# Kernel tuning notes

Measured on AMD Instinct MI355X. Metric: run time of the kernel, lower is better.

Reference implementation:

```python
import jax, jax.numpy as jnp
import numpy as np

XMIN, XMAX = -16.0, 16.0
ZMIN, ZMAX = -16.0, 16.0
SOFTCLIP_L = 5.0


def ref2mem(traj, Zs, Xs):
    # traj: (B, T, 2) cam (x, z) -> mem pixel coords
    x = (traj[..., 0] - XMIN) / ((XMAX - XMIN) / Xs) - 0.5
    z = (traj[..., 1] - ZMIN) / ((ZMAX - ZMIN) / Zs) - 0.5
    return x, z


def bilinear_sample2d(pm, x, z):
    # pm: (B, C, Z, X); x, z: (B, N) float coords -> (B, C, N)
    B, C, Zs, Xs = pm.shape
    x = jnp.clip(x, 0.0, Xs - 1.0)
    z = jnp.clip(z, 0.0, Zs - 1.0)
    x0 = jnp.floor(x).astype(jnp.int32)
    z0 = jnp.floor(z).astype(jnp.int32)
    x1 = jnp.minimum(x0 + 1, Xs - 1)
    z1 = jnp.minimum(z0 + 1, Zs - 1)
    wx = x - x0.astype(x.dtype)
    wz = z - z0.astype(z.dtype)
    pm_flat = pm.reshape(B, C, Zs * Xs)

    def gather(zi, xi):
        idx = (zi * Xs + xi)[:, None, :]  # (B,1,N)
        return jnp.take_along_axis(pm_flat, jnp.broadcast_to(idx, (B, C, idx.shape[-1])), axis=2)

    v00 = gather(z0, x0); v01 = gather(z0, x1)
    v10 = gather(z1, x0); v11 = gather(z1, x1)
    wx = wx[:, None, :]; wz = wz[:, None, :]
    return (v00 * (1 - wx) * (1 - wz) + v01 * wx * (1 - wz)
            + v10 * (1 - wx) * wz + v11 * wx * wz)


def gru_cell(x, h, W_ih, W_hh, b_ih, b_hh):
    gi = x @ W_ih.T + b_ih
    gh = h @ W_hh.T + b_hh
    i_r, i_z, i_n = jnp.split(gi, 3, axis=1)
    h_r, h_z, h_n = jnp.split(gh, 3, axis=1)
    r = jax.nn.sigmoid(i_r + h_r)
    z = jax.nn.sigmoid(i_z + h_z)
    n = jnp.tanh(i_n + r * h_n)
    return (1.0 - z) * n + z * h


def expm_softclip(sig_raw):
    B = sig_raw.shape[0]
    nrm = jnp.linalg.norm(sig_raw.reshape(B, -1), axis=1)
    denom = jax.nn.logsumexp(jnp.stack([nrm / SOFTCLIP_L, jnp.ones_like(nrm)], axis=-1), axis=-1)
    return sig_raw / denom[:, None, None]


def reference(feat_map, pred_map, noise, traj_past,
              W_ih, W_hh, b_ih, b_hh, past_W, past_b,
              W1, b1, W2, b2, W3, b3):
    B, C, Zf, Xf = feat_map.shape
    Zp, Xp = pred_map.shape[2], pred_map.shape[3]
    T_futu = noise.shape[1]
    H = W_hh.shape[1]
    eye2 = jnp.eye(2, dtype=feat_map.dtype)

    # static feature: max_pool2d k=8 s=8 + past encoding
    pooled = feat_map.reshape(B, C, Zf // 8, 8, Xf // 8, 8).max(axis=(3, 5)).reshape(B, -1)
    past_enc = traj_past.reshape(B, -1) @ past_W.T + past_b
    sta_feat = jnp.concatenate([pooled, past_enc], axis=1)  # (B, 2080)

    def step(carry, noise_t):
        hx, win = carry
        xm, zm = ref2mem(win, Zp, Xp)
        feats = bilinear_sample2d(pred_map, xm, zm).reshape(B, -1)  # (B, 3)
        dyn_feat = jnp.concatenate([feats, win.reshape(B, -1)], axis=1)  # (B, 9)
        hx = gru_cell(dyn_feat, hx, W_ih, W_hh, b_ih, b_hh)
        joint = jnp.concatenate([hx, sta_feat], axis=1)  # (B, 2112)
        h1 = jax.nn.leaky_relu(joint @ W1.T + b1)
        h2 = jax.nn.leaky_relu(h1 @ W2.T + b2)
        pred = h2 @ W3.T + b3  # (B, 6)
        mu = pred[:, :2]
        sig_raw = pred[:, 2:].reshape(B, 2, 2) + 1e-8 * eye2
        sig_raw = expm_softclip(sig_raw)
        sig = jnp.einsum('bij,bkj->bik', sig_raw, sig_raw)
        xdotdot = mu + jnp.sum(sig * noise_t[:, None, :], axis=1)
        x_next = 2.0 * win[:, -1] - win[:, -2] + xdotdot  # verlet, dt=1
        win = jnp.concatenate([win[:, 1:], x_next[:, None]], axis=1)
        return (hx, win), x_next

    hx0 = jnp.zeros((B, H), dtype=feat_map.dtype)
    (_, _), traj_futu = jax.lax.scan(step, (hx0, traj_past), jnp.swapaxes(noise, 0, 1))
    return jnp.swapaxes(traj_futu, 0, 1)  # (B, T_futu, 2)


def setup_inputs():
    key = jax.random.key(0)
    ks = jax.random.split(key, 16)
    B, C, Zf, Xf = 192, 32, 64, 64
    T_futu, T_past, H = 27, 3, 32
    d = {}
    d['feat_map'] = jax.random.normal(ks[0], (B, C, Zf, Xf), jnp.float32)
    d['pred_map'] = jax.random.normal(ks[1], (B, 1, Zf, Xf), jnp.float32)
    d['noise'] = jax.random.normal(ks[2], (B, T_futu, 2), jnp.float32)
    d['traj_past'] = jax.random.normal(ks[3], (B, T_past, 2), jnp.float32) * 4.0
    s = 0.05
    d['W_ih'] = jax.random.normal(ks[4], (3 * H, 9), jnp.float32) * s
    d['W_hh'] = jax.random.normal(ks[5], (3 * H, H), jnp.float32) * s
    d['b_ih'] = jnp.zeros((3 * H,), jnp.float32)
    d['b_hh'] = jnp.zeros((3 * H,), jnp.float32)
    d['past_W'] = jax.random.normal(ks[6], (32, T_past * 2), jnp.float32) * s
    d['past_b'] = jnp.zeros((32,), jnp.float32)
    d['W1'] = jax.random.normal(ks[7], (64, 2112), jnp.float32) * 0.02
    d['b1'] = jnp.zeros((64,), jnp.float32)
    d['W2'] = jax.random.normal(ks[8], (32, 64), jnp.float32) * s
    d['b2'] = jnp.zeros((32,), jnp.float32)
    d['W3'] = jax.random.normal(ks[9], (6, 32), jnp.float32) * s
    d['b3'] = jnp.zeros((6,), jnp.float32)
    return d
```

## Files before the change

kernel.cpp:

```cpp
#include <hip/hip_runtime.h>
#include <hip/hip_bf16.h>
#include <math.h>

typedef unsigned int u32;
typedef __fp16 f16x2 __attribute__((ext_vector_type(2)));
typedef u32 u32x4 __attribute__((ext_vector_type(4)));

#define NB    192
#define NC    32
#define TFUT  27
#define BLOB_F_OFF (NB * 64)

#if __has_builtin(__builtin_amdgcn_rcpf)
#define RCPF(x) __builtin_amdgcn_rcpf(x)
#else
#define RCPF(x) (1.0f / (x))
#endif
#if __has_builtin(__builtin_amdgcn_sqrtf)
#define SQRTF(x) __builtin_amdgcn_sqrtf(x)
#else
#define SQRTF(x) sqrtf(x)
#endif
#if __has_builtin(__builtin_amdgcn_exp2f)
#define EXP2F(x) __builtin_amdgcn_exp2f(x)
#else
#define EXP2F(x) exp2f(x)
#endif
#if __has_builtin(__builtin_amdgcn_logf)
#define LOG2F(x) __builtin_amdgcn_logf(x)
#else
#define LOG2F(x) log2f(x)
#endif

#define LDS_FENCE() asm volatile("" ::: "memory")

__device__ __forceinline__ u32 pk16(float lo, float hi) {
    auto v = __builtin_amdgcn_cvt_pkrtz(lo, hi);
    return __builtin_bit_cast(u32, v);
}
__device__ __forceinline__ float fdot2pk(u32 a, u32 b, float c) {
#if __has_builtin(__builtin_amdgcn_fdot2)
    return __builtin_amdgcn_fdot2(__builtin_bit_cast(f16x2, a),
                                  __builtin_bit_cast(f16x2, b), c, false);
#else
    f16x2 av = __builtin_bit_cast(f16x2, a), bv = __builtin_bit_cast(f16x2, b);
    return c + (float)av[0] * (float)bv[0] + (float)av[1] * (float)bv[1];
#endif
}
__device__ __forceinline__ float rdlf(float v, int lane) {
    return __int_as_float(__builtin_amdgcn_readlane(__float_as_int(v), lane));
}
__device__ __forceinline__ float dpp_xor1(float v) {
    return __int_as_float(__builtin_amdgcn_update_dpp(
        0, __float_as_int(v), 0xB1, 0xF, 0xF, true));
}
__device__ __forceinline__ float perm32hi(float v) {
    int x = __float_as_int(v), y = x;
    asm volatile("v_permlane32_swap_b32 %0, %1" : "+v"(x), "+v"(y));
    return __int_as_float(y);
}
__device__ __forceinline__ float swap32_add(float v) {
    int x = __float_as_int(v), y;
    asm volatile("v_mov_b32 %0, %1" : "=v"(y) : "v"(x));
    asm volatile("v_permlane32_swap_b32 %0, %1" : "+v"(x), "+v"(y));
    return __int_as_float(x) + __int_as_float(y);
}
__device__ __forceinline__ float row32_reduce(float v) {
    v += __int_as_float(__builtin_amdgcn_update_dpp(0, __float_as_int(v), 0x121, 0xF, 0xF, true));
    v += __int_as_float(__builtin_amdgcn_update_dpp(0, __float_as_int(v), 0x122, 0xF, 0xF, true));
    v += __int_as_float(__builtin_amdgcn_update_dpp(0, __float_as_int(v), 0x124, 0xF, 0xF, true));
    v += __int_as_float(__builtin_amdgcn_update_dpp(0, __float_as_int(v), 0x128, 0xF, 0xF, true));
    v += __int_as_float(__builtin_amdgcn_update_dpp(0, __float_as_int(v), 0x142, 0xF, 0xF, false));
    return v;
}
__device__ __forceinline__ float sigmoid_f(float x) {
    return RCPF(1.0f + EXP2F(-1.4426950408889634f * x));
}
__device__ __forceinline__ float tanh_f(float x) {
    return __builtin_fmaf(2.0f, RCPF(1.0f + EXP2F(-2.8853900817779268f * x)), -1.0f);
}

__global__ __launch_bounds__(1024) void k_static(
    const float* __restrict__ feat,
    const float* __restrict__ traj_past,
    const float* __restrict__ past_W,
    const float* __restrict__ past_b,
    const float* __restrict__ W1,
    const float* __restrict__ b1,
    const float* __restrict__ W_ih,
    const float* __restrict__ W_hh,
    const float* __restrict__ b_ih,
    const float* __restrict__ b_hh,
    const float* __restrict__ W2,
    const float* __restrict__ b2,
    const float* __restrict__ W3,
    const float* __restrict__ b3,
    float* __restrict__ ws)
{
    const int b = blockIdx.x;
    const int t = threadIdx.x;

    if (b == NB) {
        if (t >= 64) return;
        const int l = t, m2 = l & 31, h = l >> 5;
        u32* blob = reinterpret_cast<u32*>(ws) + BLOB_F_OFF + (size_t)l * 128;
        #pragma unroll
        for (int k = 0; k < 9; ++k) {
            blob[k]     = __float_as_uint(W_ih[l * 9 + k]);
            blob[9 + k] = __float_as_uint(W_ih[(64 + m2) * 9 + k]);
        }
        #pragma unroll
        for (int j = 0; j < 16; ++j) {
            blob[18 + j] = pk16(W_hh[l * 32 + 2*j],          W_hh[l * 32 + 2*j + 1]);
            blob[34 + j] = pk16(W_hh[(64 + m2) * 32 + 2*j],  W_hh[(64 + m2) * 32 + 2*j + 1]);
            blob[50 + j] = pk16(W1[(size_t)l * 2112 + 2*j],  W1[(size_t)l * 2112 + 2*j + 1]);
        }
        #pragma unroll
        for (int j = 0; j < 16; ++j)
            blob[66 + j] = pk16(W2[m2 * 64 + h * 32 + 2*j], W2[m2 * 64 + h * 32 + 2*j + 1]);
        #pragma unroll
        for (int r = 0; r < 6; ++r)
            blob[82 + r] = __float_as_uint(W3[r * 32 + m2]);
        blob[88] = blob[89] = 0u;
        blob[90] = __float_as_uint(b_ih[l]);
        blob[91] = __float_as_uint(b_hh[l]);
        blob[92] = __float_as_uint(b_ih[64 + m2]);
        blob[93] = __float_as_uint(b_hh[64 + m2]);
        blob[94] = __float_as_uint(b2[m2]);
        #pragma unroll
        for (int r = 0; r < 6; ++r) blob[95 + r] = __float_as_uint(b3[r]);
        blob[101] = blob[102] = blob[103] = 0u;
        return;
    }

    __shared__ __align__(16) float sta[2080];

    for (int it = 0; it < 2; ++it) {
        const int c    = it * 16 + (t >> 6);
        const int cell = t & 63;
        const int zi = cell >> 3, xi = cell & 7;
        const float* p = feat + ((size_t)b * NC + c) * 4096 + zi * 8 * 64 + xi * 8;
        float m = -3.402823466e38f;
        #pragma unroll
        for (int dz = 0; dz < 8; ++dz) {
            const float4 v0 = *reinterpret_cast<const float4*>(p + dz * 64);
            const float4 v1 = *reinterpret_cast<const float4*>(p + dz * 64 + 4);
            m = fmaxf(m, fmaxf(fmaxf(fmaxf(v0.x, v0.y), fmaxf(v0.z, v0.w)),
                               fmaxf(fmaxf(v1.x, v1.y), fmaxf(v1.z, v1.w))));
        }
        sta[c * 64 + cell] = m;
    }
    if (t < 32) {
        float acc = past_b[t];
        #pragma unroll
        for (int k = 0; k < 6; ++k) acc += past_W[t * 6 + k] * traj_past[b * 6 + k];
        sta[2048 + t] = acc;
    }
    __syncthreads();

    const int o = t >> 4, l = t & 15;
    const float* wrow = W1 + (size_t)o * 2112 + 32;
    float acc = 0.f;
    #pragma unroll 4
    for (int j = 0; j < 32; ++j) {
        const int k = j * 64 + l * 4;
        const float4 w = *reinterpret_cast<const float4*>(wrow + k);
        const float4 s = *reinterpret_cast<const float4*>(&sta[k]);
        acc += w.x * s.x + w.y * s.y + w.z * s.z + w.w * s.w;
    }
    if (l < 8) {
        const int k = 2048 + l * 4;
        const float4 w = *reinterpret_cast<const float4*>(wrow + k);
        const float4 s = *reinterpret_cast<const float4*>(&sta[k]);
        acc += w.x * s.x + w.y * s.y + w.z * s.z + w.w * s.w;
    }
    acc += __shfl_xor(acc, 1);
    acc += __shfl_xor(acc, 2);
    acc += __shfl_xor(acc, 4);
    acc += __shfl_xor(acc, 8);
    if (l == 0) ws[b * 64 + o] = b1[o] + acc;
}

__global__ __launch_bounds__(64, 1) void k_recur(
    const float* __restrict__ pred_map,
    const float* __restrict__ noise,
    const float* __restrict__ traj_past,
    const float* __restrict__ ws,
    float* __restrict__ out)
{
    __shared__ __align__(16) float pm[4096];
    __shared__ __align__(16) u32 hxbw[32];
    __shared__ __align__(16) u32 h1bw[32];

    const int b = blockIdx.x;
    const int l = threadIdx.x;
    const int h = l >> 5;
    const bool odd = (l & 1);

    {
        const float4* src = reinterpret_cast<const float4*>(pred_map + (size_t)b * 4096);
        float4* dst = reinterpret_cast<float4*>(pm);
        #pragma unroll
        for (int i = 0; i < 16; ++i) dst[l + i * 64] = src[l + i * 64];
    }
    const float nzreg = (l < TFUT * 2) ? noise[b * (TFUT * 2) + l] : 0.f;

    const u32* blob = reinterpret_cast<const u32*>(ws) + BLOB_F_OFF + (size_t)l * 128;
    u32x4 dv[26];
    #pragma unroll
    for (int j = 0; j < 26; ++j)
        dv[j] = reinterpret_cast<const u32x4*>(blob)[j];
#define DW(i) (dv[(i) >> 2][(i) & 3])
#define DF(i) __int_as_float((int)DW(i))

    const float sta1l = ws[b * 64 + l];

    float w[6];
    #pragma unroll
    for (int j = 0; j < 6; ++j) w[j] = traj_past[b * 6 + j];
    float hxp = 0.f;
    float Adot = 0.f, Cdot = 0.f;

    __syncthreads();

    auto bsamp = [&](float px, float pz) -> float {
        float x = __builtin_fmaf(2.0f, px, 31.5f);
        float z = __builtin_fmaf(2.0f, pz, 31.5f);
        x = fminf(fmaxf(x, 0.0f), 63.0f);
        z = fminf(fmaxf(z, 0.0f), 63.0f);
        const float xf = floorf(x), zf = floorf(z);
        const int x0 = (int)xf, z0 = (int)zf;
        const int x1 = min(x0 + 1, 63), z1 = min(z0 + 1, 63);
        const float wx = x - xf, wz = z - zf;
        const float v00 = pm[z0 * 64 + x0], v01 = pm[z0 * 64 + x1];
        const float v10 = pm[z1 * 64 + x0], v11 = pm[z1 * 64 + x1];
        const float top = v00 + wx * (v01 - v00);
        const float bot = v10 + wx * (v11 - v10);
        return top + wz * (bot - top);
    };
    float sm0 = bsamp(w[0], w[1]);
    float sm1 = bsamp(w[2], w[3]);
    float sm2 = bsamp(w[4], w[5]);

    auto pkpair = [&](float v) -> u32 {
        const float nb = dpp_xor1(v);
        const float plo = odd ? nb : v;
        const float phi = odd ? v : nb;
        return pk16(plo, phi);
    };

    for (int ts = 0; ts < TFUT; ++ts) {
        float giA = DF(90) + DF(3) * w[0] + DF(4) * w[1];
        float giB = DF(5) * w[2] + DF(6) * w[3];
        float giC = DF(7) * w[4] + DF(8) * w[5];
        float giD = DF(0) * sm0 + DF(1) * sm1 + DF(2) * sm2;
        const float gi = (giA + giB) + (giC + giD);

        float gjA = DF(92) + DF(12) * w[0] + DF(13) * w[1];
        float gjB = DF(14) * w[2] + DF(15) * w[3];
        float gjC = DF(16) * w[4] + DF(17) * w[5];
        float gjD = DF(9) * sm0 + DF(10) * sm1 + DF(11) * sm2;
        const float gi2 = (gjA + gjB) + (gjC + gjD);

        const float gs = gi + DF(91) + Adot;
        const float sg = sigmoid_f(gs);
        const float zv = perm32hi(sg);
        const float nv = tanh_f(gi2 + sg * (DF(93) + Cdot));
        const float hn = (1.0f - zv) * nv + zv * hxp;
        hxp = hn;

        hxbw[l >> 1] = pkpair(hn);
        LDS_FENCE();
        u32 hxpk[16];
        {
            const u32x4* r = reinterpret_cast<const u32x4*>(hxbw);
            const u32x4 t0 = r[0], t1 = r[1], t2 = r[2], t3 = r[3];
            #pragma unroll
            for (int q = 0; q < 4; ++q) {
                hxpk[q]      = t0[q];
                hxpk[4 + q]  = t1[q];
                hxpk[8 + q]  = t2[q];
                hxpk[12 + q] = t3[q];
            }
        }

        float D0 = 0.f, D1 = 0.f, D2 = 0.f, D3 = 0.f;
        #pragma unroll
        for (int j = 0; j < 16; j += 4) {
            D0 = fdot2pk(hxpk[j],   DW(50 + j),     D0);
            D1 = fdot2pk(hxpk[j+1], DW(50 + j + 1), D1);
            D2 = fdot2pk(hxpk[j+2], DW(50 + j + 2), D2);
            D3 = fdot2pk(hxpk[j+3], DW(50 + j + 3), D3);
        }
        const float h1a = sta1l + ((D0 + D1) + (D2 + D3));
        const float h1l = (h1a >= 0.f) ? h1a : 0.01f * h1a;

        h1bw[l >> 1] = pkpair(h1l);
        LDS_FENCE();
        u32 h1in[16];
        {
            const u32x4* r = reinterpret_cast<const u32x4*>(h1bw + (h << 4));
            const u32x4 t0 = r[0], t1 = r[1], t2 = r[2], t3 = r[3];
            #pragma unroll
            for (int q = 0; q < 4; ++q) {
                h1in[q]      = t0[q];
                h1in[4 + q]  = t1[q];
                h1in[8 + q]  = t2[q];
                h1in[12 + q] = t3[q];
            }
        }

        float A0 = 0.f, A1 = 0.f, A2 = 0.f, A3 = 0.f;
        float C0 = 0.f, C1 = 0.f, C2 = 0.f, C3 = 0.f;
        #pragma unroll
        for (int j = 0; j < 16; j += 4) {
            A0 = fdot2pk(hxpk[j],   DW(18 + j),     A0);
            A1 = fdot2pk(hxpk[j+1], DW(18 + j + 1), A1);
            A2 = fdot2pk(hxpk[j+2], DW(18 + j + 2), A2);
            A3 = fdot2pk(hxpk[j+3], DW(18 + j + 3), A3);
            C0 = fdot2pk(hxpk[j],   DW(34 + j),     C0);
            C1 = fdot2pk(hxpk[j+1], DW(34 + j + 1), C1);
            C2 = fdot2pk(hxpk[j+2], DW(34 + j + 2), C2);
            C3 = fdot2pk(hxpk[j+3], DW(34 + j + 3), C3);
        }
        Adot = (A0 + A1) + (A2 + A3);
        Cdot = (C0 + C1) + (C2 + C3);

        float P0 = 0.f, P1 = 0.f, P2 = 0.f, P3 = 0.f;
        #pragma unroll
        for (int j = 0; j < 16; j += 4) {
            P0 = fdot2pk(h1in[j],   DW(66 + j),     P0);
            P1 = fdot2pk(h1in[j+1], DW(66 + j + 1), P1);
            P2 = fdot2pk(h1in[j+2], DW(66 + j + 2), P2);
            P3 = fdot2pk(h1in[j+3], DW(66 + j + 3), P3);
        }
        const float Pown = (P0 + P1) + (P2 + P3);
        const float h2a = DF(94) + swap32_add(Pown);
        const float h2l = (h2a >= 0.f) ? h2a : 0.01f * h2a;

        const float q0 = row32_reduce(DF(82) * h2l);
        const float q1 = row32_reduce(DF(83) * h2l);
        const float q2 = row32_reduce(DF(84) * h2l);
        const float q3 = row32_reduce(DF(85) * h2l);
        const float q4 = row32_reduce(DF(86) * h2l);
        const float q5 = row32_reduce(DF(87) * h2l);

        const float pv0 = rdlf(q0, 16) + DF(95);
        const float pv1 = rdlf(q1, 16) + DF(96);
        const float pv2 = rdlf(q2, 16) + DF(97);
        const float pv3 = rdlf(q3, 16) + DF(98);
        const float pv4 = rdlf(q4, 16) + DF(99);
        const float pv5 = rdlf(q5, 16) + DF(100);

        const float s00 = pv2 + 1e-8f, s01 = pv3;
        const float s10 = pv4,          s11 = pv5 + 1e-8f;
        const float p00 = s00 * s00 + s01 * s01;
        const float p01 = s00 * s10 + s01 * s11;
        const float p11 = s10 * s10 + s11 * s11;
        const float nrm = SQRTF(p00 + p11);
        const float arg = nrm * 0.2f;
        const float mmx = fmaxf(arg, 1.0f);
        const float dd  = fabsf(arg - 1.0f);
        const float den = mmx + 0.6931471805599453f *
                          LOG2F(1.0f + EXP2F(-1.4426950408889634f * dd));
        const float inv  = RCPF(den);
        const float inv2 = inv * inv;

        const float nnx = rdlf(nzreg, 2 * ts);
        const float nny = rdlf(nzreg, 2 * ts + 1);
        const float xd0 = pv0 + nnx * ((p00 + p01) * inv2);
        const float xd1 = pv1 + nny * ((p01 + p11) * inv2);
        const float nx0 = 2.0f * w[4] - w[2] + xd0;
        const float nx1 = 2.0f * w[5] - w[3] + xd1;

        if (l == 0) {
            float2 o; o.x = nx0; o.y = nx1;
            *reinterpret_cast<float2*>(out + ((size_t)b * TFUT + ts) * 2) = o;
        }

        w[0] = w[2]; w[1] = w[3];
        w[2] = w[4]; w[3] = w[5];
        w[4] = nx0;  w[5] = nx1;
        sm0 = sm1; sm1 = sm2;
        sm2 = bsamp(nx0, nx1);
    }
#undef DW
#undef DF
}

extern "C" void kernel_launch(void* const* d_in, const int* in_sizes, int n_in,
                              void* d_out, int out_size, void* d_ws, size_t ws_size,
                              hipStream_t stream) {
    const float* feat      = (const float*)d_in[0];
    const float* pred_map  = (const float*)d_in[1];
    const float* noise     = (const float*)d_in[2];
    const float* traj_past = (const float*)d_in[3];
    const float* W_ih      = (const float*)d_in[4];
    const float* W_hh      = (const float*)d_in[5];
    const float* b_ih      = (const float*)d_in[6];
    const float* b_hh      = (const float*)d_in[7];
    const float* past_W    = (const float*)d_in[8];
    const float* past_b    = (const float*)d_in[9];
    const float* W1        = (const float*)d_in[10];
    const float* b1        = (const float*)d_in[11];
    const float* W2        = (const float*)d_in[12];
    const float* b2        = (const float*)d_in[13];
    const float* W3        = (const float*)d_in[14];
    const float* b3        = (const float*)d_in[15];
    float* outp = (float*)d_out;
    float* ws   = (float*)d_ws;

    k_static<<<dim3(NB + 1), dim3(1024), 0, stream>>>(
        feat, traj_past, past_W, past_b, W1, b1,
        W_ih, W_hh, b_ih, b_hh, W2, b2, W3, b3, ws);
    k_recur<<<dim3(NB), dim3(64), 0, stream>>>(pred_map, noise, traj_past, ws, outp);
}
```

Before: 44.92 us.

## Interleave two batch recurrences per wavefront in the recurrent kernel

The recurrent kernel now processes two batch elements per 64-lane block, interleaving their independent GRU/MLP steps so each one's latency-bound dependency chain can overlap with the other's. The grid is halved to 96 blocks and LDS use roughly doubles to hold two prediction maps. With 192 single-wave blocks already fitting on the device's CUs, this trades parallelism across CUs for instruction-level parallelism within one wave, and adds register pressure.

```diff
diff --git a/kernel.cpp b/kernel.cpp
--- a/kernel.cpp
+++ b/kernel.cpp
@@ -9,6 +9,7 @@
 #define NB    192
 #define NC    32
 #define TFUT  27
+#define NPAIR 96
 #define BLOB_F_OFF (NB * 64)
 
 #if __has_builtin(__builtin_amdgcn_rcpf)
@@ -188,22 +189,27 @@
     const float* __restrict__ ws,
     float* __restrict__ out)
 {
-    __shared__ __align__(16) float pm[4096];
-    __shared__ __align__(16) u32 hxbw[32];
-    __shared__ __align__(16) u32 h1bw[32];
-
-    const int b = blockIdx.x;
+    __shared__ __align__(16) float pm_0[4096];
+    __shared__ __align__(16) float pm_1[4096];
+    __shared__ __align__(16) u32 hxbw_0[32], hxbw_1[32];
+    __shared__ __align__(16) u32 h1bw_0[32], h1bw_1[32];
+
     const int l = threadIdx.x;
     const int h = l >> 5;
     const bool odd = (l & 1);
+    const int bA = blockIdx.x;
+    const int bB = blockIdx.x + NPAIR;
 
     {
-        const float4* src = reinterpret_cast<const float4*>(pred_map + (size_t)b * 4096);
-        float4* dst = reinterpret_cast<float4*>(pm);
-        #pragma unroll
-        for (int i = 0; i < 16; ++i) dst[l + i * 64] = src[l + i * 64];
-    }
-    const float nzreg = (l < TFUT * 2) ? noise[b * (TFUT * 2) + l] : 0.f;
+        const float4* s0 = reinterpret_cast<const float4*>(pred_map + (size_t)bA * 4096);
+        const float4* s1 = reinterpret_cast<const float4*>(pred_map + (size_t)bB * 4096);
+        float4* d0 = reinterpret_cast<float4*>(pm_0);
+        float4* d1 = reinterpret_cast<float4*>(pm_1);
+        #pragma unroll
+        for (int i = 0; i < 16; ++i) { d0[l + i * 64] = s0[l + i * 64]; d1[l + i * 64] = s1[l + i * 64]; }
+    }
+    const float nz_0 = (l < TFUT * 2) ? noise[bA * (TFUT * 2) + l] : 0.f;
+    const float nz_1 = (l < TFUT * 2) ? noise[bB * (TFUT * 2) + l] : 0.f;
 
     const u32* blob = reinterpret_cast<const u32*>(ws) + BLOB_F_OFF + (size_t)l * 128;
     u32x4 dv[26];
@@ -213,17 +219,18 @@
 #define DW(i) (dv[(i) >> 2][(i) & 3])
 #define DF(i) __int_as_float((int)DW(i))
 
-    const float sta1l = ws[b * 64 + l];
-
-    float w[6];
+    const float sta1_0 = ws[bA * 64 + l];
+    const float sta1_1 = ws[bB * 64 + l];
+
+    float w_0[6], w_1[6];
     #pragma unroll
-    for (int j = 0; j < 6; ++j) w[j] = traj_past[b * 6 + j];
-    float hxp = 0.f;
-    float Adot = 0.f, Cdot = 0.f;
+    for (int j = 0; j < 6; ++j) { w_0[j] = traj_past[bA * 6 + j]; w_1[j] = traj_past[bB * 6 + j]; }
+    float hxp_0 = 0.f, Adot_0 = 0.f, Cdot_0 = 0.f;
+    float hxp_1 = 0.f, Adot_1 = 0.f, Cdot_1 = 0.f;
 
     __syncthreads();
 
-    auto bsamp = [&](float px, float pz) -> float {
+    auto bsamp = [&](const float* pmp, float px, float pz) -> float {
         float x = __builtin_fmaf(2.0f, px, 31.5f);
         float z = __builtin_fmaf(2.0f, pz, 31.5f);
         x = fminf(fmaxf(x, 0.0f), 63.0f);
@@ -232,15 +239,18 @@
         const int x0 = (int)xf, z0 = (int)zf;
         const int x1 = min(x0 + 1, 63), z1 = min(z0 + 1, 63);
         const float wx = x - xf, wz = z - zf;
-        const float v00 = pm[z0 * 64 + x0], v01 = pm[z0 * 64 + x1];
-        const float v10 = pm[z1 * 64 + x0], v11 = pm[z1 * 64 + x1];
+        const float v00 = pmp[z0 * 64 + x0], v01 = pmp[z0 * 64 + x1];
+        const float v10 = pmp[z1 * 64 + x0], v11 = pmp[z1 * 64 + x1];
         const float top = v00 + wx * (v01 - v00);
         const float bot = v10 + wx * (v11 - v10);
         return top + wz * (bot - top);
     };
-    float sm0 = bsamp(w[0], w[1]);
-    float sm1 = bsamp(w[2], w[3]);
-    float sm2 = bsamp(w[4], w[5]);
+    float sm0_0 = bsamp(pm_0, w_0[0], w_0[1]);
+    float sm1_0 = bsamp(pm_0, w_0[2], w_0[3]);
+    float sm2_0 = bsamp(pm_0, w_0[4], w_0[5]);
+    float sm0_1 = bsamp(pm_1, w_1[0], w_1[1]);
+    float sm1_1 = bsamp(pm_1, w_1[2], w_1[3]);
+    float sm2_1 = bsamp(pm_1, w_1[4], w_1[5]);
 
     auto pkpair = [&](float v) -> u32 {
         const float nb = dpp_xor1(v);
@@ -249,141 +259,141 @@
         return pk16(plo, phi);
     };
 
+#define GATES(S) { \
+    float giA = DF(90) + DF(3) * w_##S[0] + DF(4) * w_##S[1]; \
+    float giB = DF(5) * w_##S[2] + DF(6) * w_##S[3]; \
+    float giC = DF(7) * w_##S[4] + DF(8) * w_##S[5]; \
+    float giD = DF(0) * sm0_##S + DF(1) * sm1_##S + DF(2) * sm2_##S; \
+    const float gi = (giA + giB) + (giC + giD); \
+    float gjA = DF(92) + DF(12) * w_##S[0] + DF(13) * w_##S[1]; \
+    float gjB = DF(14) * w_##S[2] + DF(15) * w_##S[3]; \
+    float gjC = DF(16) * w_##S[4] + DF(17) * w_##S[5]; \
+    float gjD = DF(9) * sm0_##S + DF(10) * sm1_##S + DF(11) * sm2_##S; \
+    const float gi2 = (gjA + gjB) + (gjC + gjD); \
+    const float gs = gi + DF(91) + Adot_##S; \
+    const float sg = sigmoid_f(gs); \
+    const float zv = perm32hi(sg); \
+    const float nv = tanh_f(gi2 + sg * (DF(93) + Cdot_##S)); \
+    const float hn = (1.0f - zv) * nv + zv * hxp_##S; \
+    hxp_##S = hn; \
+    hxbw_##S[l >> 1] = pkpair(hn); }
+
+#define READHX(S) \
+    u32 hxpk_##S[16]; \
+    { const u32x4* r = reinterpret_cast<const u32x4*>(hxbw_##S); \
+      const u32x4 t0 = r[0], t1 = r[1], t2 = r[2], t3 = r[3]; \
+      _Pragma("unroll") for (int q = 0; q < 4; ++q) { \
+          hxpk_##S[q] = t0[q]; hxpk_##S[4+q] = t1[q]; \
+          hxpk_##S[8+q] = t2[q]; hxpk_##S[12+q] = t3[q]; } }
+
+#define H1DOTS(S) \
+    float h1l_##S; \
+    { float D0 = 0.f, D1 = 0.f, D2 = 0.f, D3 = 0.f; \
+      _Pragma("unroll") for (int j = 0; j < 16; j += 4) { \
+          D0 = fdot2pk(hxpk_##S[j],   DW(50 + j),     D0); \
+          D1 = fdot2pk(hxpk_##S[j+1], DW(50 + j + 1), D1); \
+          D2 = fdot2pk(hxpk_##S[j+2], DW(50 + j + 2), D2); \
+          D3 = fdot2pk(hxpk_##S[j+3], DW(50 + j + 3), D3); } \
+      const float h1a = sta1_##S + ((D0 + D1) + (D2 + D3)); \
+      h1l_##S = (h1a >= 0.f) ? h1a : 0.01f * h1a; \
+      h1bw_##S[l >> 1] = pkpair(h1l_##S); }
+
+#define READH1(S) \
+    u32 h1in_##S[16]; \
+    { const u32x4* r = reinterpret_cast<const u32x4*>(h1bw_##S + (h << 4)); \
+      const u32x4 t0 = r[0], t1 = r[1], t2 = r[2], t3 = r[3]; \
+      _Pragma("unroll") for (int q = 0; q < 4; ++q) { \
+          h1in_##S[q] = t0[q]; h1in_##S[4+q] = t1[q]; \
+          h1in_##S[8+q] = t2[q]; h1in_##S[12+q] = t3[q]; } }
+
+#define ADCD(S) { \
+    float A0 = 0.f, A1 = 0.f, A2 = 0.f, A3 = 0.f; \
+    float C0 = 0.f, C1 = 0.f, C2 = 0.f, C3 = 0.f; \
+    _Pragma("unroll") for (int j = 0; j < 16; j += 4) { \
+        A0 = fdot2pk(hxpk_##S[j],   DW(18 + j),     A0); \
+        A1 = fdot2pk(hxpk_##S[j+1], DW(18 + j + 1), A1); \
+        A2 = fdot2pk(hxpk_##S[j+2], DW(18 + j + 2), A2); \
+        A3 = fdot2pk(hxpk_##S[j+3], DW(18 + j + 3), A3); \
+        C0 = fdot2pk(hxpk_##S[j],   DW(34 + j),     C0); \
+        C1 = fdot2pk(hxpk_##S[j+1], DW(34 + j + 1), C1); \
+        C2 = fdot2pk(hxpk_##S[j+2], DW(34 + j + 2), C2); \
+        C3 = fdot2pk(hxpk_##S[j+3], DW(34 + j + 3), C3); } \
+    Adot_##S = (A0 + A1) + (A2 + A3); \
+    Cdot_##S = (C0 + C1) + (C2 + C3); }
+
+#define TAIL(S, BEXP, PM) { \
+    float P0 = 0.f, P1 = 0.f, P2 = 0.f, P3 = 0.f; \
+    _Pragma("unroll") for (int j = 0; j < 16; j += 4) { \
+        P0 = fdot2pk(h1in_##S[j],   DW(66 + j),     P0); \
+        P1 = fdot2pk(h1in_##S[j+1], DW(66 + j + 1), P1); \
+        P2 = fdot2pk(h1in_##S[j+2], DW(66 + j + 2), P2); \
+        P3 = fdot2pk(h1in_##S[j+3], DW(66 + j + 3), P3); } \
+    const float Pown = (P0 + P1) + (P2 + P3); \
+    const float h2a = DF(94) + swap32_add(Pown); \
+    const float h2l = (h2a >= 0.f) ? h2a : 0.01f * h2a; \
+    const float q0 = row32_reduce(DF(82) * h2l); \
+    const float q1 = row32_reduce(DF(83) * h2l); \
+    const float q2 = row32_reduce(DF(84) * h2l); \
+    const float q3 = row32_reduce(DF(85) * h2l); \
+    const float q4 = row32_reduce(DF(86) * h2l); \
+    const float q5 = row32_reduce(DF(87) * h2l); \
+    const float pv0 = rdlf(q0, 16) + DF(95); \
+    const float pv1 = rdlf(q1, 16) + DF(96); \
+    const float pv2 = rdlf(q2, 16) + DF(97); \
+    const float pv3 = rdlf(q3, 16) + DF(98); \
+    const float pv4 = rdlf(q4, 16) + DF(99); \
+    const float pv5 = rdlf(q5, 16) + DF(100); \
+    const float s00 = pv2 + 1e-8f, s01 = pv3; \
+    const float s10 = pv4,          s11 = pv5 + 1e-8f; \
+    const float p00 = s00 * s00 + s01 * s01; \
+    const float p01 = s00 * s10 + s01 * s11; \
+    const float p11 = s10 * s10 + s11 * s11; \
+    const float nrm = SQRTF(p00 + p11); \
+    const float arg = nrm * 0.2f; \
+    const float mmx = fmaxf(arg, 1.0f); \
+    const float dd  = fabsf(arg - 1.0f); \
+    const float den = mmx + 0.6931471805599453f * \
+                      LOG2F(1.0f + EXP2F(-1.4426950408889634f * dd)); \
+    const float inv  = RCPF(den); \
+    const float inv2 = inv * inv; \
+    const float nnx = rdlf(nz_##S, 2 * ts); \
+    const float nny = rdlf(nz_##S, 2 * ts + 1); \
+    const float xd0 = pv0 + nnx * ((p00 + p01) * inv2); \
+    const float xd1 = pv1 + nny * ((p01 + p11) * inv2); \
+    const float nx0 = 2.0f * w_##S[4] - w_##S[2] + xd0; \
+    const float nx1 = 2.0f * w_##S[5] - w_##S[3] + xd1; \
+    if (l == 0) { \
+        float2 o; o.x = nx0; o.y = nx1; \
+        *reinterpret_cast<float2*>(out + ((size_t)(BEXP) * TFUT + ts) * 2) = o; \
+    } \
+    w_##S[0] = w_##S[2]; w_##S[1] = w_##S[3]; \
+    w_##S[2] = w_##S[4]; w_##S[3] = w_##S[5]; \
+    w_##S[4] = nx0;      w_##S[5] = nx1; \
+    sm0_##S = sm1_##S; sm1_##S = sm2_##S; \
+    sm2_##S = bsamp(PM, nx0, nx1); }
+
     for (int ts = 0; ts < TFUT; ++ts) {
-        float giA = DF(90) + DF(3) * w[0] + DF(4) * w[1];
-        float giB = DF(5) * w[2] + DF(6) * w[3];
-        float giC = DF(7) * w[4] + DF(8) * w[5];
-        float giD = DF(0) * sm0 + DF(1) * sm1 + DF(2) * sm2;
-        const float gi = (giA + giB) + (giC + giD);
-
-        float gjA = DF(92) + DF(12) * w[0] + DF(13) * w[1];
-        float gjB = DF(14) * w[2] + DF(15) * w[3];
-        float gjC = DF(16) * w[4] + DF(17) * w[5];
-        float gjD = DF(9) * sm0 + DF(10) * sm1 + DF(11) * sm2;
-        const float gi2 = (gjA + gjB) + (gjC + gjD);
-
-        const float gs = gi + DF(91) + Adot;
-        const float sg = sigmoid_f(gs);
-        const float zv = perm32hi(sg);
-        const float nv = tanh_f(gi2 + sg * (DF(93) + Cdot));
-        const float hn = (1.0f - zv) * nv + zv * hxp;
-        hxp = hn;
-
-        hxbw[l >> 1] = pkpair(hn);
+        GATES(0)
+        GATES(1)
         LDS_FENCE();
-        u32 hxpk[16];
-        {
-            const u32x4* r = reinterpret_cast<const u32x4*>(hxbw);
-            const u32x4 t0 = r[0], t1 = r[1], t2 = r[2], t3 = r[3];
-            #pragma unroll
-            for (int q = 0; q < 4; ++q) {
-                hxpk[q]      = t0[q];
-                hxpk[4 + q]  = t1[q];
-                hxpk[8 + q]  = t2[q];
-                hxpk[12 + q] = t3[q];
-            }
-        }
-
-        float D0 = 0.f, D1 = 0.f, D2 = 0.f, D3 = 0.f;
-        #pragma unroll
-        for (int j = 0; j < 16; j += 4) {
-            D0 = fdot2pk(hxpk[j],   DW(50 + j),     D0);
-            D1 = fdot2pk(hxpk[j+1], DW(50 + j + 1), D1);
-            D2 = fdot2pk(hxpk[j+2], DW(50 + j + 2), D2);
-            D3 = fdot2pk(hxpk[j+3], DW(50 + j + 3), D3);
-        }
-        const float h1a = sta1l + ((D0 + D1) + (D2 + D3));
-        const float h1l = (h1a >= 0.f) ? h1a : 0.01f * h1a;
-
-        h1bw[l >> 1] = pkpair(h1l);
+        READHX(0)
+        READHX(1)
+        H1DOTS(0)
+        H1DOTS(1)
         LDS_FENCE();
-        u32 h1in[16];
-        {
-            const u32x4* r = reinterpret_cast<const u32x4*>(h1bw + (h << 4));
-            const u32x4 t0 = r[0], t1 = r[1], t2 = r[2], t3 = r[3];
-            #pragma unroll
-            for (int q = 0; q < 4; ++q) {
-                h1in[q]      = t0[q];
-                h1in[4 + q]  = t1[q];
-                h1in[8 + q]  = t2[q];
-                h1in[12 + q] = t3[q];
-            }
-        }
-
-        float A0 = 0.f, A1 = 0.f, A2 = 0.f, A3 = 0.f;
-        float C0 = 0.f, C1 = 0.f, C2 = 0.f, C3 = 0.f;
-        #pragma unroll
-        for (int j = 0; j < 16; j += 4) {
-            A0 = fdot2pk(hxpk[j],   DW(18 + j),     A0);
-            A1 = fdot2pk(hxpk[j+1], DW(18 + j + 1), A1);
-            A2 = fdot2pk(hxpk[j+2], DW(18 + j + 2), A2);
-            A3 = fdot2pk(hxpk[j+3], DW(18 + j + 3), A3);
-            C0 = fdot2pk(hxpk[j],   DW(34 + j),     C0);
-            C1 = fdot2pk(hxpk[j+1], DW(34 + j + 1), C1);
-            C2 = fdot2pk(hxpk[j+2], DW(34 + j + 2), C2);
-            C3 = fdot2pk(hxpk[j+3], DW(34 + j + 3), C3);
-        }
-        Adot = (A0 + A1) + (A2 + A3);
-        Cdot = (C0 + C1) + (C2 + C3);
-
-        float P0 = 0.f, P1 = 0.f, P2 = 0.f, P3 = 0.f;
-        #pragma unroll
-        for (int j = 0; j < 16; j += 4) {
-            P0 = fdot2pk(h1in[j],   DW(66 + j),     P0);
-            P1 = fdot2pk(h1in[j+1], DW(66 + j + 1), P1);
-            P2 = fdot2pk(h1in[j+2], DW(66 + j + 2), P2);
-            P3 = fdot2pk(h1in[j+3], DW(66 + j + 3), P3);
-        }
-        const float Pown = (P0 + P1) + (P2 + P3);
-        const float h2a = DF(94) + swap32_add(Pown);
-        const float h2l = (h2a >= 0.f) ? h2a : 0.01f * h2a;
-
-        const float q0 = row32_reduce(DF(82) * h2l);
-        const float q1 = row32_reduce(DF(83) * h2l);
-        const float q2 = row32_reduce(DF(84) * h2l);
-        const float q3 = row32_reduce(DF(85) * h2l);
-        const float q4 = row32_reduce(DF(86) * h2l);
-        const float q5 = row32_reduce(DF(87) * h2l);
-
-        const float pv0 = rdlf(q0, 16) + DF(95);
-        const float pv1 = rdlf(q1, 16) + DF(96);
-        const float pv2 = rdlf(q2, 16) + DF(97);
-        const float pv3 = rdlf(q3, 16) + DF(98);
-        const float pv4 = rdlf(q4, 16) + DF(99);
-        const float pv5 = rdlf(q5, 16) + DF(100);
-
-        const float s00 = pv2 + 1e-8f, s01 = pv3;
-        const float s10 = pv4,          s11 = pv5 + 1e-8f;
-        const float p00 = s00 * s00 + s01 * s01;
-        const float p01 = s00 * s10 + s01 * s11;
-        const float p11 = s10 * s10 + s11 * s11;
-        const float nrm = SQRTF(p00 + p11);
-        const float arg = nrm * 0.2f;
-        const float mmx = fmaxf(arg, 1.0f);
-        const float dd  = fabsf(arg - 1.0f);
-        const float den = mmx + 0.6931471805599453f *
-                          LOG2F(1.0f + EXP2F(-1.4426950408889634f * dd));
-        const float inv  = RCPF(den);
-        const float inv2 = inv * inv;
-
-        const float nnx = rdlf(nzreg, 2 * ts);
-        const float nny = rdlf(nzreg, 2 * ts + 1);
-        const float xd0 = pv0 + nnx * ((p00 + p01) * inv2);
-        const float xd1 = pv1 + nny * ((p01 + p11) * inv2);
-        const float nx0 = 2.0f * w[4] - w[2] + xd0;
-        const float nx1 = 2.0f * w[5] - w[3] + xd1;
-
-        if (l == 0) {
-            float2 o; o.x = nx0; o.y = nx1;
-            *reinterpret_cast<float2*>(out + ((size_t)b * TFUT + ts) * 2) = o;
-        }
-
-        w[0] = w[2]; w[1] = w[3];
-        w[2] = w[4]; w[3] = w[5];
-        w[4] = nx0;  w[5] = nx1;
-        sm0 = sm1; sm1 = sm2;
-        sm2 = bsamp(nx0, nx1);
-    }
+        READH1(0)
+        READH1(1)
+        ADCD(0)
+        ADCD(1)
+        TAIL(0, bA, pm_0)
+        TAIL(1, bB, pm_1)
+    }
+#undef GATES
+#undef READHX
+#undef H1DOTS
+#undef READH1
+#undef ADCD
+#undef TAIL
 #undef DW
 #undef DF
 }
@@ -413,5 +423,5 @@
     k_static<<<dim3(NB + 1), dim3(1024), 0, stream>>>(
         feat, traj_past, past_W, past_b, W1, b1,
         W_ih, W_hh, b_ih, b_hh, W2, b2, W3, b3, ws);
-    k_recur<<<dim3(NB), dim3(64), 0, stream>>>(pred_map, noise, traj_past, ws, outp);
-}
+    k_recur<<<dim3(NPAIR), dim3(64), 0, stream>>>(pred_map, noise, traj_past, ws, outp);
+}
```

After: 59.27 us. 31.9% more time.
